# Performance work log

Measured on AMD Instinct MI355X. Metric: run time of the kernel, lower is better.

Reference implementation:

```python
import jax, jax.numpy as jnp
import numpy as np

EPS = 1e-5
CHUNK = 256
N_LAYERS = 4
D_MODEL = 1024
D_INNER = 2048
D_HEAD = 64
N_HEADS = 32
D_STATE = 64
D_CONV = 4
CONV_DIM = D_INNER + 2 * D_STATE  # ngroups=1
D_IN_PROJ = 2 * D_INNER + 2 * D_STATE + N_HEADS


def silu(x):
    return x * jax.nn.sigmoid(x)


def rmsnorm(x, w):
    return x * jax.lax.rsqrt(jnp.mean(x * x, axis=-1, keepdims=True) + EPS) * w


def segsum(x):
    # x: [..., T] -> [..., T, T] lower-triangular segment sums, -inf above diag
    T = x.shape[-1]
    cs = jnp.cumsum(x, axis=-1)
    ss = cs[..., :, None] - cs[..., None, :]
    mask = jnp.tril(jnp.ones((T, T), dtype=bool))
    return jnp.where(mask, ss, -jnp.inf)


def ssd(X, A, B, C, chunk):
    # X: [b,l,h,p] (already scaled by dt), A: [b,l,h] (= dt * A_head), B,C: [b,l,n] (ngroups=1)
    b, l, h, p = X.shape
    c = l // chunk
    X = X.reshape(b, c, chunk, h, p)
    A = A.reshape(b, c, chunk, h).transpose(0, 3, 1, 2)  # [b,h,c,l]
    B = B.reshape(b, c, chunk, -1)
    C = C.reshape(b, c, chunk, -1)
    Acs = jnp.cumsum(A, axis=-1)  # [b,h,c,l]
    # intra-chunk (diagonal blocks)
    Lm = jnp.exp(segsum(A))  # [b,h,c,l,l]
    Y_diag = jnp.einsum('bcln,bcsn,bhcls,bcshp->bclhp', C, B, Lm, X)
    # chunk end states
    decay_states = jnp.exp(Acs[..., -1:] - Acs)  # [b,h,c,l]
    states = jnp.einsum('bcln,bhcl,bclhp->bchpn', B, decay_states, X)
    # inter-chunk recurrence (c is small -> dense segsum over chunks)
    A_last = jnp.pad(Acs[..., -1], ((0, 0), (0, 0), (1, 0)))  # [b,h,c+1]
    decay_chunk = jnp.exp(segsum(A_last))  # [b,h,c+1,c+1]
    states = jnp.concatenate([jnp.zeros_like(states[:, :1]), states], axis=1)
    new_states = jnp.einsum('bhzc,bchpn->bzhpn', decay_chunk, states)
    states = new_states[:, :-1]  # state entering each chunk
    Y_off = jnp.einsum('bcln,bchpn,bhcl->bclhp', C, states, jnp.exp(Acs))
    return (Y_diag + Y_off).reshape(b, l, h, p)


def mamba2_layer(x, in_w, conv_w, conv_b, dt_bias, A_log, D, gnorm_w, out_w):
    b, l, _ = x.shape
    zxbcdt = jnp.einsum('bld,ed->ble', x, in_w)  # [b,l,D_IN_PROJ]
    z = zxbcdt[..., :D_INNER]
    xBC = zxbcdt[..., D_INNER:D_INNER + CONV_DIM]
    dt = zxbcdt[..., D_INNER + CONV_DIM:]  # [b,l,h]
    # depthwise causal conv1d + silu
    xpad = jnp.pad(xBC, ((0, 0), (D_CONV - 1, 0), (0, 0)))
    xconv = conv_b
    for k in range(D_CONV):
        xconv = xconv + xpad[:, k:k + l, :] * conv_w[:, k]
    xBC = silu(xconv)
    x_in = xBC[..., :D_INNER]
    B = xBC[..., D_INNER:D_INNER + D_STATE]
    C = xBC[..., D_INNER + D_STATE:]
    dt = jax.nn.softplus(dt + dt_bias)  # [b,l,h]
    A = -jnp.exp(A_log)  # [h]
    X = x_in.reshape(b, l, N_HEADS, D_HEAD)
    y = ssd(X * dt[..., None], dt * A, B, C, CHUNK)
    y = y + D[None, None, :, None] * X
    y = y.reshape(b, l, D_INNER)
    y = rmsnorm(y * silu(z), gnorm_w)
    return jnp.einsum('ble,de->bld', y, out_w)


def setup_inputs() -> dict:
    key = jax.random.key(0)
    ks = jax.random.split(key, 8)
    x = jax.random.normal(ks[0], (2, 2048, D_MODEL), dtype=jnp.float32)
    in_proj_w = jax.random.normal(ks[1], (N_LAYERS, D_IN_PROJ, D_MODEL), dtype=jnp.float32) * 0.02
    conv_w = jax.random.uniform(ks[2], (N_LAYERS, CONV_DIM, D_CONV), dtype=jnp.float32, minval=-0.5, maxval=0.5)
    conv_b = jnp.zeros((N_LAYERS, CONV_DIM), dtype=jnp.float32)
    A_log = jnp.log(jax.random.uniform(ks[3], (N_LAYERS, N_HEADS), dtype=jnp.float32, minval=1.0, maxval=16.0))
    dt0 = jax.random.uniform(ks[4], (N_LAYERS, N_HEADS), dtype=jnp.float32, minval=0.001, maxval=0.1)
    dt_bias = dt0 + jnp.log(-jnp.expm1(-dt0))  # inverse softplus
    D = jnp.ones((N_LAYERS, N_HEADS), dtype=jnp.float32)
    gnorm_w = jnp.ones((N_LAYERS, D_INNER), dtype=jnp.float32)
    out_proj_w = jax.random.normal(ks[5], (N_LAYERS, D_MODEL, D_INNER), dtype=jnp.float32) * 0.02
    rms_w = jnp.ones((N_LAYERS, D_MODEL), dtype=jnp.float32)
    return {"x": x, "in_proj_w": in_proj_w, "conv_w": conv_w, "conv_b": conv_b,
            "dt_bias": dt_bias, "A_log": A_log, "D": D, "gnorm_w": gnorm_w,
            "out_proj_w": out_proj_w, "rms_w": rms_w}


def reference(x, in_proj_w, conv_w, conv_b, dt_bias, A_log, D, gnorm_w, out_proj_w, rms_w):
    for i in range(N_LAYERS):
        x = x + mamba2_layer(rmsnorm(x, rms_w[i]), in_proj_w[i], conv_w[i], conv_b[i],
                             dt_bias[i], A_log[i], D[i], gnorm_w[i], out_proj_w[i])
    return x
```

## Files before the change

kernel.cpp:

```cpp
#include <hip/hip_runtime.h>
#include <cmath>

#define BATCH 2
#define LSEQ 2048
#define DMODEL 1024
#define DINNER 2048
#define NHEADS 32
#define DHEAD 64
#define DSTATE 64
#define DCONV 4
#define CONVDIM (DINNER + 2*DSTATE)
#define DINPROJ (2*DINNER + 2*DSTATE + NHEADS)
#define DINPROJ_PAD 4352
#define CHUNKSZ 256
#define NCHUNK (LSEQ/CHUNKSZ)
#define MROWS (BATCH*LSEQ)
#define EPSF 1e-5f

typedef __attribute__((ext_vector_type(8))) short shortx8;
typedef __attribute__((ext_vector_type(4))) short shortx4;
typedef __attribute__((ext_vector_type(4))) float floatx4;

__device__ __forceinline__ ushort f2bf(float f) {
  unsigned u = __float_as_uint(f);
  unsigned r = (u + 0x7fffu + ((u >> 16) & 1u)) >> 16;
  return (ushort)r;
}
__device__ __forceinline__ float bf2f(ushort b) {
  return __uint_as_float(((unsigned)b) << 16);
}

__device__ __forceinline__ shortx8 pack8(float4 a, float4 b) {
  shortx8 r;
  r[0] = (short)f2bf(a.x); r[1] = (short)f2bf(a.y);
  r[2] = (short)f2bf(a.z); r[3] = (short)f2bf(a.w);
  r[4] = (short)f2bf(b.x); r[5] = (short)f2bf(b.y);
  r[6] = (short)f2bf(b.z); r[7] = (short)f2bf(b.w);
  return r;
}

__device__ __forceinline__ void async_load16(const void* g, void* l) {
  __builtin_amdgcn_global_load_lds(
      (const __attribute__((address_space(1))) void*)g,
      (__attribute__((address_space(3))) void*)l, 16, 0, 0);
}

__device__ __forceinline__ float block_reduce_sum_256(float v, float* sb) {
  for (int off = 32; off > 0; off >>= 1) v += __shfl_down(v, off, 64);
  int lane = threadIdx.x & 63, wid = threadIdx.x >> 6;
  if (lane == 0) sb[wid] = v;
  __syncthreads();
  return sb[0] + sb[1] + sb[2] + sb[3];
}

__global__ __launch_bounds__(256) void cvt_bf16_k(const float* __restrict__ src,
                                                  ushort* __restrict__ dst,
                                                  size_t n_src, size_t n_dst) {
  size_t i = (size_t)blockIdx.x * 256 + threadIdx.x;
  if (i >= n_dst) return;
  float v = (i < n_src) ? src[i] : 0.f;
  dst[i] = f2bf(v);
}

__global__ __launch_bounds__(256) void cvt_w_all(const float* __restrict__ in_w,
                                                 const float* __restrict__ out_w,
                                                 ushort* __restrict__ in_bf,
                                                 ushort* __restrict__ out_bf) {
  unsigned g = (blockIdx.x * 256u + threadIdx.x) * 8u;
  const unsigned PL = (unsigned)DINPROJ_PAD * DMODEL;
  const unsigned n1 = 4u * PL;
  const unsigned n2 = 4u * DMODEL * DINNER;
  if (g < n1) {
    unsigned layer = g / PL, rem = g % PL;
    unsigned row = rem / DMODEL, col = rem % DMODEL;
    shortx8 o;
    if (row < DINPROJ) {
      const float* sp = in_w + ((size_t)layer * DINPROJ + row) * DMODEL + col;
      float4 a = *(const float4*)sp;
      float4 b = *(const float4*)(sp + 4);
      o = pack8(a, b);
    } else {
#pragma unroll
      for (int j = 0; j < 8; j++) o[j] = 0;
    }
    *(shortx8*)(in_bf + g) = o;
  } else if (g < n1 + n2) {
    unsigned j = g - n1;
    const float* sp = out_w + j;
    float4 a = *(const float4*)sp;
    float4 b = *(const float4*)(sp + 4);
    *(shortx8*)(out_bf + j) = pack8(a, b);
  }
}

__global__ __launch_bounds__(256) void rmsnorm_k(const float* __restrict__ x,
                                                 const float* __restrict__ w,
                                                 ushort* __restrict__ out) {
  __shared__ float sb[4];
  int r = blockIdx.x;
  const float* xr = x + (size_t)r * DMODEL;
  ushort* orow = out + (size_t)r * DMODEL;
  int c0 = threadIdx.x * 4;
  float4 v4 = *(const float4*)(xr + c0);
  float ssq = v4.x * v4.x + v4.y * v4.y + v4.z * v4.z + v4.w * v4.w;
  float s = block_reduce_sum_256(ssq, sb);
  float sc = rsqrtf(s / (float)DMODEL + EPSF);
  float4 w4 = *(const float4*)(w + c0);
  shortx4 o;
  o[0] = (short)f2bf(v4.x * sc * w4.x);
  o[1] = (short)f2bf(v4.y * sc * w4.y);
  o[2] = (short)f2bf(v4.z * sc * w4.z);
  o[3] = (short)f2bf(v4.w * sc * w4.w);
  *(shortx4*)(orow + c0) = o;
}

__device__ __forceinline__ void stage_tile(const ushort* __restrict__ A,
                                           const ushort* __restrict__ B,
                                           char* lb, int m0, int n0, int K, int k0,
                                           int wid, int rA, int sA) {
#pragma unroll
  for (int rd = 0; rd < 2; rd++) {
    int r = rd * 64 + rA;
    int sl = sA ^ ((r ^ (r >> 2)) & 3);
    async_load16(A + (size_t)(m0 + r) * K + (k0 + sl * 8), lb + rd * 4096 + wid * 1024);
  }
#pragma unroll
  for (int rd = 0; rd < 2; rd++) {
    int r = rd * 64 + rA;
    int sl = sA ^ ((r ^ (r >> 2)) & 3);
    async_load16(B + (size_t)(n0 + r) * K + (k0 + sl * 8), lb + 8192 + rd * 4096 + wid * 1024);
  }
}

__global__ __launch_bounds__(256, 3) void gemm_nt_mfma_pipe(
    const ushort* __restrict__ A, const ushort* __restrict__ B,
    ushort* __restrict__ Cbf, int M, int N, int K,
    int nbx, int rw, int rh) {
  __shared__ __align__(16) char lds[3][16384];
  int tid = threadIdx.x;
  int wid = tid >> 6, lane = tid & 63;
  int quad = lane >> 4, lrow = lane & 15;

  int d = blockIdx.x;
  int xcd = d & 7, wi = d >> 3;
  int ra = nbx / rw;
  int rn = xcd % ra, rm = xcd / ra;
  int bx = rn * rw + wi % rw;
  int by = rm * rh + wi / rw;

  int m0 = by * 128, n0 = bx * 128;
  int wm = (wid >> 1) * 64, wn = (wid & 1) * 64;
  int rA = tid >> 2, sA = tid & 3;

  floatx4 acc[4][4];
#pragma unroll
  for (int i = 0; i < 4; i++)
#pragma unroll
    for (int j = 0; j < 4; j++) acc[i][j] = (floatx4){0.f, 0.f, 0.f, 0.f};

  int NT = K >> 5;
#pragma unroll
  for (int t = 0; t < 2; t++)
    stage_tile(A, B, lds[t], m0, n0, K, t * 32, wid, rA, sA);

  int cur = 0, sb = 2;
  for (int t = 0; t < NT; t++) {
    if (t < NT - 1) asm volatile("s_waitcnt vmcnt(4)" ::: "memory");
    else            asm volatile("s_waitcnt vmcnt(0)" ::: "memory");
    __builtin_amdgcn_s_barrier();
    __builtin_amdgcn_sched_barrier(0);
    if (t + 2 < NT) {
      stage_tile(A, B, lds[sb], m0, n0, K, (t + 2) * 32, wid, rA, sA);
      sb = (sb == 2) ? 0 : sb + 1;
    }

    const char* Ab = lds[cur];
    const char* Bb = Ab + 8192;
    cur = (cur == 2) ? 0 : cur + 1;
    shortx8 af[4], bfr[4];
#pragma unroll
    for (int i = 0; i < 4; i++) {
      int r = wm + i * 16 + lrow;
      af[i] = *(const shortx8*)(Ab + r * 64 + ((quad ^ ((r ^ (r >> 2)) & 3)) << 4));
    }
#pragma unroll
    for (int j = 0; j < 4; j++) {
      int r = wn + j * 16 + lrow;
      bfr[j] = *(const shortx8*)(Bb + r * 64 + ((quad ^ ((r ^ (r >> 2)) & 3)) << 4));
    }
    __builtin_amdgcn_s_setprio(1);
#pragma unroll
    for (int i = 0; i < 4; i++)
#pragma unroll
      for (int j = 0; j < 4; j++)
        acc[i][j] = __builtin_amdgcn_mfma_f32_16x16x32_bf16(af[i], bfr[j], acc[i][j], 0, 0, 0);
    __builtin_amdgcn_s_setprio(0);
  }

#pragma unroll
  for (int i = 0; i < 4; i++) {
    int r0 = m0 + wm + i * 16 + quad * 4;
#pragma unroll
    for (int j = 0; j < 4; j++) {
      int n = n0 + wn + j * 16 + lrow;
      if (n < N)
#pragma unroll
        for (int r = 0; r < 4; r++)
          Cbf[(size_t)(r0 + r) * N + n] = f2bf(acc[i][j][r]);
    }
  }
}

__device__ __forceinline__ void stage_tile64(const ushort* __restrict__ A,
                                             const ushort* __restrict__ B,
                                             char* lb, int m0, int n0, int K, int k0,
                                             int wid, int rA, int sA) {
#pragma unroll
  for (int rd = 0; rd < 2; rd++) {
    int r = rd * 64 + rA;
    int sl = sA ^ ((r ^ (r >> 2)) & 3);
    async_load16(A + (size_t)(m0 + r) * K + (k0 + sl * 8), lb + rd * 4096 + wid * 1024);
  }
  {
    int r = rA;
    int sl = sA ^ ((r ^ (r >> 2)) & 3);
    async_load16(B + (size_t)(n0 + r) * K + (k0 + sl * 8), lb + 8192 + wid * 1024);
  }
}

__global__ __launch_bounds__(256, 2) void gemm_nt_64(
    const ushort* __restrict__ A, const ushort* __restrict__ B,
    float* __restrict__ C, const float* __restrict__ resid,
    int M, int N, int K, int nbx, int rw, int rh) {
  __shared__ __align__(16) char lds[3][12288];
  int tid = threadIdx.x;
  int wid = tid >> 6, lane = tid & 63;
  int quad = lane >> 4, lrow = lane & 15;

  int d = blockIdx.x;
  int xcd = d & 7, wi = d >> 3;
  int ra = nbx / rw;
  int rn = xcd % ra, rm = xcd / ra;
  int bx = rn * rw + wi % rw;
  int by = rm * rh + wi / rw;

  int m0 = by * 128, n0 = bx * 64;
  int wm = (wid >> 1) * 64, wn = (wid & 1) * 32;
  int rA = tid >> 2, sA = tid & 3;

  floatx4 acc[4][2];
#pragma unroll
  for (int i = 0; i < 4; i++)
#pragma unroll
    for (int j = 0; j < 2; j++) acc[i][j] = (floatx4){0.f, 0.f, 0.f, 0.f};

  int NT = K >> 5;
#pragma unroll
  for (int t = 0; t < 2; t++)
    stage_tile64(A, B, lds[t], m0, n0, K, t * 32, wid, rA, sA);

  int cur = 0, sb = 2;
  for (int t = 0; t < NT; t++) {
    if (t < NT - 1) asm volatile("s_waitcnt vmcnt(3)" ::: "memory");
    else            asm volatile("s_waitcnt vmcnt(0)" ::: "memory");
    __builtin_amdgcn_s_barrier();
    __builtin_amdgcn_sched_barrier(0);
    if (t + 2 < NT) {
      stage_tile64(A, B, lds[sb], m0, n0, K, (t + 2) * 32, wid, rA, sA);
      sb = (sb == 2) ? 0 : sb + 1;
    }

    const char* Ab = lds[cur];
    const char* Bb = Ab + 8192;
    cur = (cur == 2) ? 0 : cur + 1;
    shortx8 af[4], bfr[2];
#pragma unroll
    for (int i = 0; i < 4; i++) {
      int r = wm + i * 16 + lrow;
      af[i] = *(const shortx8*)(Ab + r * 64 + ((quad ^ ((r ^ (r >> 2)) & 3)) << 4));
    }
#pragma unroll
    for (int j = 0; j < 2; j++) {
      int r = wn + j * 16 + lrow;
      bfr[j] = *(const shortx8*)(Bb + r * 64 + ((quad ^ ((r ^ (r >> 2)) & 3)) << 4));
    }
    __builtin_amdgcn_s_setprio(1);
#pragma unroll
    for (int i = 0; i < 4; i++)
#pragma unroll
      for (int j = 0; j < 2; j++)
        acc[i][j] = __builtin_amdgcn_mfma_f32_16x16x32_bf16(af[i], bfr[j], acc[i][j], 0, 0, 0);
    __builtin_amdgcn_s_setprio(0);
  }

  bool hasR = (resid != nullptr);
#pragma unroll
  for (int i = 0; i < 4; i++) {
    int r0 = m0 + wm + i * 16 + quad * 4;
#pragma unroll
    for (int j = 0; j < 2; j++) {
      int n = n0 + wn + j * 16 + lrow;
#pragma unroll
      for (int r = 0; r < 4; r++) {
        size_t idx = (size_t)(r0 + r) * N + n;
        float v = acc[i][j][r];
        if (hasR) v += resid[idx];
        C[idx] = v;
      }
    }
  }
}

__global__ __launch_bounds__(256) void convcum_k(const ushort* __restrict__ zxbf,
                                                 const float* __restrict__ cw,
                                                 const float* __restrict__ cb,
                                                 ushort* __restrict__ xbf,
                                                 const float* __restrict__ dt_bias,
                                                 const float* __restrict__ A_log,
                                                 float* __restrict__ dt_sp,
                                                 float* __restrict__ dtA_cs) {
  __shared__ float buf[256];
  int tid = threadIdx.x;
  if (blockIdx.x < MROWS / 8) {
    int r0 = blockIdx.x * 8;
    int bstart = r0 & ~(LSEQ - 1);
#pragma unroll
    for (int rep = 0; rep < 2; rep++) {
      int ch;
      if (rep == 0) ch = tid * 8;
      else { if (tid >= (CONVDIM - 2048) / 8) break; ch = 2048 + tid * 8; }
      float wv[8][4], bias[8];
#pragma unroll
      for (int j = 0; j < 8; j++) {
        float4 w4 = *(const float4*)(cw + (ch + j) * 4);
        wv[j][0] = w4.x; wv[j][1] = w4.y; wv[j][2] = w4.z; wv[j][3] = w4.w;
        bias[j] = cb[ch + j];
      }
      float xw[11][8];
#pragma unroll
      for (int wr = 0; wr < 11; wr++) {
        int rr = r0 - 3 + wr;
        if (rr < bstart) {
#pragma unroll
          for (int j = 0; j < 8; j++) xw[wr][j] = 0.f;
        } else {
          shortx8 v = *(const shortx8*)(zxbf + (size_t)rr * DINPROJ + DINNER + ch);
#pragma unroll
          for (int j = 0; j < 8; j++) xw[wr][j] = bf2f((ushort)v[j]);
        }
      }
#pragma unroll
      for (int o = 0; o < 8; o++) {
        shortx8 ov;
#pragma unroll
        for (int j = 0; j < 8; j++) {
          float acc = bias[j];
#pragma unroll
          for (int k = 0; k < 4; k++) acc += xw[o + k][j] * wv[j][k];
          float s = acc / (1.f + expf(-acc));
          ov[j] = (short)f2bf(s);
        }
        *(shortx8*)(xbf + (size_t)(r0 + o) * CONVDIM + ch) = ov;
      }
    }
  } else {
    int bid = blockIdx.x - MROWS / 8;
    int h = bid & 31, c = (bid >> 5) & 7, b = bid >> 8;
    int l = tid;
    float Aneg = -expf(A_log[h]);
    int row = b * LSEQ + c * CHUNKSZ + l;
    float v = bf2f(zxbf[(size_t)row * DINPROJ + DINNER + CONVDIM + h]) + dt_bias[h];
    float dtv = (v > 20.f) ? v : log1pf(expf(v));
    dt_sp[row * 32 + h] = dtv;
    buf[l] = dtv * Aneg;
    __syncthreads();
    for (int off = 1; off < 256; off <<= 1) {
      float add = (l >= off) ? buf[l - off] : 0.f;
      __syncthreads();
      buf[l] += add;
      __syncthreads();
    }
    dtA_cs[(size_t)bid * CHUNKSZ + l] = buf[l];
  }
}

#define ST_STRIDE 72
__global__ __launch_bounds__(256) void states_mfma(const ushort* __restrict__ xbf,
                                                   const float* __restrict__ dt_sp,
                                                   const float* __restrict__ dtA_cs,
                                                   float* __restrict__ st_raw) {
  __shared__ ushort XT[64 * ST_STRIDE];
  __shared__ ushort BT[64 * ST_STRIDE];
  __shared__ float wrow[64];
  int bid = blockIdx.x;
  int h = bid & 31, c = (bid >> 5) & 7, b = bid >> 8;
  int tid = threadIdx.x;
  int w = tid >> 6, lane = tid & 63;
  int quad = lane >> 4, lrow = lane & 15;
  int cbase = bid * CHUNKSZ;
  int rowbase = b * LSEQ + c * CHUNKSZ;
  float T = dtA_cs[cbase + CHUNKSZ - 1];
  floatx4 acc[4];
  for (int jt = 0; jt < 4; jt++) acc[jt] = (floatx4){0.f, 0.f, 0.f, 0.f};
  int row_l = tid >> 2, seg = tid & 3;
  for (int lt = 0; lt < 4; lt++) {
    __syncthreads();
    if (tid < 64) {
      int row = rowbase + lt * 64 + tid;
      wrow[tid] = dt_sp[row * 32 + h] * __expf(T - dtA_cs[cbase + lt * 64 + tid]);
    }
    __syncthreads();
    {
      int row = rowbase + lt * 64 + row_l;
      const ushort* bp = xbf + (size_t)row * CONVDIM + DINNER + seg * 16;
      const ushort* xp = xbf + (size_t)row * CONVDIM + h * DHEAD + seg * 16;
      shortx8 b0 = *(const shortx8*)bp;
      shortx8 b1 = *(const shortx8*)(bp + 8);
      shortx8 x0 = *(const shortx8*)xp;
      shortx8 x1 = *(const shortx8*)(xp + 8);
      float wv = wrow[row_l];
#pragma unroll
      for (int j = 0; j < 8; j++) {
        int c0 = seg * 16 + j;
        int c1 = c0 + 8;
        int k0 = ((c0 >> 1) & 7) << 3;
        int k1 = ((c1 >> 1) & 7) << 3;
        BT[c0 * ST_STRIDE + (row_l ^ k0)] = (ushort)b0[j];
        BT[c1 * ST_STRIDE + (row_l ^ k1)] = (ushort)b1[j];
        XT[c0 * ST_STRIDE + (row_l ^ k0)] = f2bf(bf2f((ushort)x0[j]) * wv);
        XT[c1 * ST_STRIDE + (row_l ^ k1)] = f2bf(bf2f((ushort)x1[j]) * wv);
      }
    }
    __syncthreads();
    int arow = w * 16 + lrow;
    int akey = ((arow >> 1) & 7) << 3;
    for (int kk = 0; kk < 64; kk += 32) {
      shortx8 af = *(const shortx8*)&XT[arow * ST_STRIDE + ((kk + quad * 8) ^ akey)];
      for (int jt = 0; jt < 4; jt++) {
        int brow = jt * 16 + lrow;
        int bkey = ((brow >> 1) & 7) << 3;
        shortx8 bf = *(const shortx8*)&BT[brow * ST_STRIDE + ((kk + quad * 8) ^ bkey)];
        acc[jt] = __builtin_amdgcn_mfma_f32_16x16x32_bf16(af, bf, acc[jt], 0, 0, 0);
      }
    }
  }
  size_t base = (size_t)bid * (DHEAD * DSTATE);
  for (int jt = 0; jt < 4; jt++) {
    int n = jt * 16 + lrow;
    for (int r = 0; r < 4; r++) {
      int p = w * 16 + quad * 4 + r;
      st_raw[base + (size_t)p * 64 + n] = acc[jt][r];
    }
  }
}

__global__ __launch_bounds__(256) void scan_k(float* __restrict__ st,
                                              const float* __restrict__ dtA_cs) {
  int bid = blockIdx.x;
  int seg = bid & 3, h = (bid >> 2) & 31, b = bid >> 7;
  int tid = threadIdx.x;
  int off = seg * 1024;
  float s[4];
  for (int i = 0; i < 4; i++) s[i] = 0.f;
  for (int c = 0; c < NCHUNK; c++) {
    int g = (b * NCHUNK + c) * 32 + h;
    float dec = expf(dtA_cs[(size_t)g * CHUNKSZ + CHUNKSZ - 1]);
    size_t base = (size_t)g * (DHEAD * DSTATE) + off;
    for (int i = 0; i < 4; i++) {
      int idx = tid + i * 256;
      float raw = st[base + idx];
      st[base + idx] = s[i];
      s[i] = s[i] * dec + raw;
    }
  }
}

#define BS_STRIDE 72
#define XT_STRIDE 68
#define PW_STRIDE 72
__global__ __launch_bounds__(256) void ydiag_mfma(const ushort* __restrict__ xbf,
                                                  const float* __restrict__ dt_sp,
                                                  const float* __restrict__ dtA_cs,
                                                  const float* __restrict__ st_in,
                                                  ushort* __restrict__ Y) {
  __shared__ ushort Bs[64 * BS_STRIDE];
  __shared__ ushort XsT[64 * XT_STRIDE];
  __shared__ ushort Pw[4 * 16 * PW_STRIDE];
  __shared__ float cs[256];
  int tid = threadIdx.x;
  int w = tid >> 6, lane = tid & 63;
  int quad = lane >> 4, lrow = lane & 15;
  int bid = blockIdx.x;
  int lt = bid & 3, h = (bid >> 2) & 31, c = (bid >> 7) & 7, b = bid >> 10;
  int g = (b * NCHUNK + c) * 32 + h;
  int cbase = g * CHUNKSZ;
  int rowbase = b * LSEQ + c * CHUNKSZ;

  cs[tid] = dtA_cs[cbase + tid];
  __syncthreads();

  int mrow = lt * 64 + w * 16;
  float csl[4];
  for (int r = 0; r < 4; r++) csl[r] = cs[mrow + quad * 4 + r];

  shortx8 Cf[2];
  {
    const ushort* cp = xbf + (size_t)(rowbase + mrow + lrow) * CONVDIM + DINNER + DSTATE;
    for (int q = 0; q < 2; q++)
      Cf[q] = *(const shortx8*)(cp + q * 32 + quad * 8);
  }

  floatx4 acc[4];
  for (int jt = 0; jt < 4; jt++) acc[jt] = (floatx4){0.f, 0.f, 0.f, 0.f};
  const float* stp = st_in + (size_t)g * (DHEAD * DSTATE);
  for (int q = 0; q < 2; q++) {
    for (int jt = 0; jt < 4; jt++) {
      const float* sp = stp + (size_t)(jt * 16 + lrow) * 64 + q * 32 + quad * 8;
      shortx8 sf = pack8(*(const float4*)sp, *(const float4*)(sp + 4));
      acc[jt] = __builtin_amdgcn_mfma_f32_16x16x32_bf16(Cf[q], sf, acc[jt], 0, 0, 0);
    }
  }
  for (int jt = 0; jt < 4; jt++)
    for (int r = 0; r < 4; r++) acc[jt][r] *= __expf(csl[r]);

  ushort* myP = Pw + w * 16 * PW_STRIDE;
  int row_l = tid >> 2, seg = tid & 3;
  for (int st = 0; st <= lt; st++) {
    __syncthreads();
    {
      int row = rowbase + st * 64 + row_l;
      const ushort* bp = xbf + (size_t)row * CONVDIM + DINNER + seg * 16;
      const ushort* xp = xbf + (size_t)row * CONVDIM + h * DHEAD + seg * 16;
      shortx8 b0 = *(const shortx8*)bp;
      shortx8 b1 = *(const shortx8*)(bp + 8);
      shortx8 x0 = *(const shortx8*)xp;
      shortx8 x1 = *(const shortx8*)(xp + 8);
      float dtv = dt_sp[row * 32 + h];
      *(shortx8*)&Bs[row_l * BS_STRIDE + seg * 16] = b0;
      *(shortx8*)&Bs[row_l * BS_STRIDE + seg * 16 + 8] = b1;
#pragma unroll
      for (int j = 0; j < 8; j++) {
        int c0 = seg * 16 + j;
        XsT[c0 * XT_STRIDE + row_l]       = f2bf(bf2f((ushort)x0[j]) * dtv);
        XsT[(c0 + 8) * XT_STRIDE + row_l] = f2bf(bf2f((ushort)x1[j]) * dtv);
      }
    }
    __syncthreads();
    for (int jt = 0; jt < 4; jt++) {
      floatx4 s = (floatx4){0.f, 0.f, 0.f, 0.f};
      for (int q = 0; q < 2; q++) {
        shortx8 bfr = *(const shortx8*)&Bs[(jt * 16 + lrow) * BS_STRIDE + q * 32 + quad * 8];
        s = __builtin_amdgcn_mfma_f32_16x16x32_bf16(Cf[q], bfr, s, 0, 0, 0);
      }
      int scol = st * 64 + jt * 16 + lrow;
      float css = cs[scol];
      for (int r = 0; r < 4; r++) {
        int l = mrow + quad * 4 + r;
        float v = (scol <= l) ? s[r] * __expf(csl[r] - css) : 0.f;
        myP[(quad * 4 + r) * PW_STRIDE + jt * 16 + lrow] = f2bf(v);
      }
    }
    shortx8 pf[2];
    for (int q = 0; q < 2; q++)
      pf[q] = *(const shortx8*)&myP[lrow * PW_STRIDE + q * 32 + quad * 8];
    for (int jt = 0; jt < 4; jt++) {
      for (int q = 0; q < 2; q++) {
        const ushort* xp = &XsT[(jt * 16 + lrow) * XT_STRIDE + q * 32 + quad * 8];
        shortx4 lo = *(const shortx4*)xp;
        shortx4 hi = *(const shortx4*)(xp + 4);
        shortx8 xf = __builtin_shufflevector(lo, hi, 0, 1, 2, 3, 4, 5, 6, 7);
        acc[jt] = __builtin_amdgcn_mfma_f32_16x16x32_bf16(pf[q], xf, acc[jt], 0, 0, 0);
      }
    }
  }
  int growb = rowbase + mrow + quad * 4;
  for (int jt = 0; jt < 4; jt++)
    for (int r = 0; r < 4; r++)
      Y[(size_t)(growb + r) * DINNER + h * DHEAD + jt * 16 + lrow] = f2bf(acc[jt][r]);
}

__global__ __launch_bounds__(256) void gatenorm_k(const ushort* __restrict__ Ybf,
                                                  const ushort* __restrict__ zxbf,
                                                  const ushort* __restrict__ xbf,
                                                  const float* __restrict__ Dvec,
                                                  const float* __restrict__ gw,
                                                  ushort* __restrict__ obf) {
  __shared__ float sb[4];
  int r = blockIdx.x;
  int c0 = threadIdx.x * 8;
  const ushort* yr = Ybf + (size_t)r * DINNER;
  const ushort* zr = zxbf + (size_t)r * DINPROJ;
  const ushort* xr = xbf + (size_t)r * CONVDIM;
  ushort* orow = obf + (size_t)r * DINNER;
  shortx8 y8 = *(const shortx8*)(yr + c0);
  shortx8 z8 = *(const shortx8*)(zr + c0);
  shortx8 x8 = *(const shortx8*)(xr + c0);
  float Dv = Dvec[threadIdx.x >> 3];
  float t[8]; float ssq = 0.f;
#pragma unroll
  for (int i = 0; i < 8; i++) {
    float z = bf2f((ushort)z8[i]);
    float yv = bf2f((ushort)y8[i]) + Dv * bf2f((ushort)x8[i]);
    float gv = yv * (z / (1.f + expf(-z)));
    t[i] = gv;
    ssq += gv * gv;
  }
  float s = block_reduce_sum_256(ssq, sb);
  float sc = rsqrtf(s / (float)DINNER + EPSF);
  float4 g0 = *(const float4*)(gw + c0);
  float4 g1 = *(const float4*)(gw + c0 + 4);
  shortx8 o;
  o[0] = (short)f2bf(t[0] * sc * g0.x); o[1] = (short)f2bf(t[1] * sc * g0.y);
  o[2] = (short)f2bf(t[2] * sc * g0.z); o[3] = (short)f2bf(t[3] * sc * g0.w);
  o[4] = (short)f2bf(t[4] * sc * g1.x); o[5] = (short)f2bf(t[5] * sc * g1.y);
  o[6] = (short)f2bf(t[6] * sc * g1.z); o[7] = (short)f2bf(t[7] * sc * g1.w);
  *(shortx8*)(orow + c0) = o;
}

extern "C" void kernel_launch(void* const* d_in, const int* in_sizes, int n_in,
                              void* d_out, int out_size, void* d_ws, size_t ws_size,
                              hipStream_t stream) {
  const float* x_in     = (const float*)d_in[0];
  const float* in_w     = (const float*)d_in[1];
  const float* conv_w   = (const float*)d_in[2];
  const float* conv_b   = (const float*)d_in[3];
  const float* dt_bias  = (const float*)d_in[4];
  const float* A_log    = (const float*)d_in[5];
  const float* Dvec     = (const float*)d_in[6];
  const float* gnorm_w  = (const float*)d_in[7];
  const float* out_w    = (const float*)d_in[8];
  const float* rms_w    = (const float*)d_in[9];
  float* out = (float*)d_out;

  float* ws = (float*)d_ws;
  size_t o = 0;
  float* x_cur  = ws + o; o += (size_t)MROWS * DMODEL;
  ushort* zx_bf = (ushort*)(ws + o); o += (size_t)MROWS * DINPROJ / 2;
  ushort* xbf   = (ushort*)(ws + o); o += (size_t)MROWS * CONVDIM / 2;
  float* dt_sp  = ws + o; o += (size_t)MROWS * NHEADS;
  float* dtA_cs = ws + o; o += (size_t)BATCH * NCHUNK * NHEADS * CHUNKSZ;
  float* st     = ws + o; o += (size_t)BATCH * NCHUNK * NHEADS * DHEAD * DSTATE;
  ushort* Ybf   = (ushort*)(ws + o); o += (size_t)MROWS * DINNER / 2;
  ushort* act_bf = (ushort*)(ws + o); o += (size_t)MROWS * DINNER / 2;
  size_t base_f = o;

  size_t inw_f  = (size_t)4 * DINPROJ_PAD * DMODEL / 2;
  size_t outw_f = (size_t)4 * DMODEL * DINNER / 2;
  bool hoist = ws_size >= (base_f + inw_f + outw_f) * sizeof(float);

  ushort* in_bf_all = (ushort*)(ws + base_f);
  ushort* out_bf_all = (ushort*)(ws + base_f + inw_f);
  ushort* w_bf_fb = (ushort*)(ws + base_f);

  hipMemcpyAsync(x_cur, x_in, (size_t)MROWS * DMODEL * sizeof(float),
                 hipMemcpyDeviceToDevice, stream);

  if (hoist) {
    unsigned ntot = (4u * DINPROJ_PAD * DMODEL + 4u * DMODEL * DINNER) / 8u;
    cvt_w_all<<<(ntot + 255) / 256, 256, 0, stream>>>(in_w, out_w, in_bf_all, out_bf_all);
  }

  for (int i = 0; i < 4; i++) {
    const float* conv_w_i = conv_w  + (size_t)i * CONVDIM * DCONV;
    const float* conv_b_i = conv_b  + (size_t)i * CONVDIM;
    const float* dtb_i    = dt_bias + (size_t)i * NHEADS;
    const float* Alog_i   = A_log   + (size_t)i * NHEADS;
    const float* D_i      = Dvec    + (size_t)i * NHEADS;
    const float* gw_i     = gnorm_w + (size_t)i * DINNER;
    const float* rms_w_i  = rms_w   + (size_t)i * DMODEL;

    const ushort* w1_bf;
    const ushort* w2_bf;
    if (hoist) {
      w1_bf = in_bf_all  + (size_t)i * DINPROJ_PAD * DMODEL;
      w2_bf = out_bf_all + (size_t)i * DMODEL * DINNER;
    } else {
      size_t ns = (size_t)DINPROJ * DMODEL, nd = (size_t)DINPROJ_PAD * DMODEL;
      cvt_bf16_k<<<(nd + 255) / 256, 256, 0, stream>>>(
          in_w + (size_t)i * DINPROJ * DMODEL, w_bf_fb, ns, nd);
      w1_bf = w_bf_fb;
      w2_bf = w_bf_fb;
    }

    rmsnorm_k<<<MROWS, 256, 0, stream>>>(x_cur, rms_w_i, act_bf);
    gemm_nt_mfma_pipe<<<(DINPROJ_PAD / 128) * (MROWS / 128), 256, 0, stream>>>(
        act_bf, w1_bf, zx_bf, MROWS, DINPROJ, DMODEL, DINPROJ_PAD / 128, 17, 8);
    convcum_k<<<MROWS / 8 + BATCH * NCHUNK * NHEADS, 256, 0, stream>>>(
        zx_bf, conv_w_i, conv_b_i, xbf, dtb_i, Alog_i, dt_sp, dtA_cs);
    states_mfma<<<BATCH * NCHUNK * NHEADS, 256, 0, stream>>>(xbf, dt_sp, dtA_cs, st);
    scan_k<<<BATCH * NHEADS * 4, 256, 0, stream>>>(st, dtA_cs);
    ydiag_mfma<<<BATCH * NCHUNK * NHEADS * 4, 256, 0, stream>>>(
        xbf, dt_sp, dtA_cs, st, Ybf);
    gatenorm_k<<<MROWS, 256, 0, stream>>>(Ybf, zx_bf, xbf, D_i, gw_i, act_bf);
    if (!hoist) {
      size_t ns = (size_t)DMODEL * DINNER;
      cvt_bf16_k<<<(ns + 255) / 256, 256, 0, stream>>>(
          out_w + (size_t)i * DMODEL * DINNER, (ushort*)w_bf_fb, ns, ns);
    }
    float* outC = (i == 3) ? out : x_cur;
    gemm_nt_64<<<(MROWS / 128) * (DMODEL / 64), 256, 0, stream>>>(
        act_bf, w2_bf, outC, x_cur, MROWS, DMODEL, DINNER, DMODEL / 64, 8, 8);
  }
}
```

Baseline: 868.6 us.

## Merge ydiag row tiles into one block per chunk-head to reuse B/X staging

The ydiag kernel previously launched four blocks per (batch, chunk, head), one per 64-row tile, each restaging B and dt-scaled X tiles into shared memory. Now one block processes all four row tiles, loading each B/X source tile once and applying it to every causal row tile. This removes redundant global loads and conversions but quadruples accumulator registers (64 floatx4 values plus C fragments), cuts the grid from 2048 to 512 blocks, and serialises more work per block, which may lower occupancy.

```diff
diff --git a/kernel.cpp b/kernel.cpp
--- a/kernel.cpp
+++ b/kernel.cpp
@@ -491,7 +491,7 @@
   int w = tid >> 6, lane = tid & 63;
   int quad = lane >> 4, lrow = lane & 15;
   int bid = blockIdx.x;
-  int lt = bid & 3, h = (bid >> 2) & 31, c = (bid >> 7) & 7, b = bid >> 10;
+  int h = bid & 31, c = (bid >> 5) & 7, b = bid >> 8;
   int g = (b * NCHUNK + c) * 32 + h;
   int cbase = g * CHUNKSZ;
   int rowbase = b * LSEQ + c * CHUNKSZ;
@@ -499,33 +499,43 @@
   cs[tid] = dtA_cs[cbase + tid];
   __syncthreads();
 
-  int mrow = lt * 64 + w * 16;
-  float csl[4];
-  for (int r = 0; r < 4; r++) csl[r] = cs[mrow + quad * 4 + r];
-
-  shortx8 Cf[2];
-  {
+  shortx8 Cf[4][2];
+  float csl[4][4];
+  floatx4 acc[4][4];
+#pragma unroll
+  for (int mt = 0; mt < 4; mt++) {
+    int mrow = mt * 64 + w * 16;
+#pragma unroll
+    for (int r = 0; r < 4; r++) csl[mt][r] = cs[mrow + quad * 4 + r];
     const ushort* cp = xbf + (size_t)(rowbase + mrow + lrow) * CONVDIM + DINNER + DSTATE;
-    for (int q = 0; q < 2; q++)
-      Cf[q] = *(const shortx8*)(cp + q * 32 + quad * 8);
-  }
-
-  floatx4 acc[4];
-  for (int jt = 0; jt < 4; jt++) acc[jt] = (floatx4){0.f, 0.f, 0.f, 0.f};
+#pragma unroll
+    for (int q = 0; q < 2; q++) Cf[mt][q] = *(const shortx8*)(cp + q * 32 + quad * 8);
+#pragma unroll
+    for (int jt = 0; jt < 4; jt++) acc[mt][jt] = (floatx4){0.f, 0.f, 0.f, 0.f};
+  }
+
   const float* stp = st_in + (size_t)g * (DHEAD * DSTATE);
+#pragma unroll
   for (int q = 0; q < 2; q++) {
+#pragma unroll
     for (int jt = 0; jt < 4; jt++) {
       const float* sp = stp + (size_t)(jt * 16 + lrow) * 64 + q * 32 + quad * 8;
       shortx8 sf = pack8(*(const float4*)sp, *(const float4*)(sp + 4));
-      acc[jt] = __builtin_amdgcn_mfma_f32_16x16x32_bf16(Cf[q], sf, acc[jt], 0, 0, 0);
-    }
-  }
-  for (int jt = 0; jt < 4; jt++)
-    for (int r = 0; r < 4; r++) acc[jt][r] *= __expf(csl[r]);
+#pragma unroll
+      for (int mt = 0; mt < 4; mt++)
+        acc[mt][jt] = __builtin_amdgcn_mfma_f32_16x16x32_bf16(Cf[mt][q], sf, acc[mt][jt], 0, 0, 0);
+    }
+  }
+#pragma unroll
+  for (int mt = 0; mt < 4; mt++)
+#pragma unroll
+    for (int jt = 0; jt < 4; jt++)
+#pragma unroll
+      for (int r = 0; r < 4; r++) acc[mt][jt][r] *= __expf(csl[mt][r]);
 
   ushort* myP = Pw + w * 16 * PW_STRIDE;
   int row_l = tid >> 2, seg = tid & 3;
-  for (int st = 0; st <= lt; st++) {
+  for (int st = 0; st < 4; st++) {
     __syncthreads();
     {
       int row = rowbase + st * 64 + row_l;
@@ -546,37 +556,53 @@
       }
     }
     __syncthreads();
-    for (int jt = 0; jt < 4; jt++) {
-      floatx4 s = (floatx4){0.f, 0.f, 0.f, 0.f};
-      for (int q = 0; q < 2; q++) {
-        shortx8 bfr = *(const shortx8*)&Bs[(jt * 16 + lrow) * BS_STRIDE + q * 32 + quad * 8];
-        s = __builtin_amdgcn_mfma_f32_16x16x32_bf16(Cf[q], bfr, s, 0, 0, 0);
-      }
-      int scol = st * 64 + jt * 16 + lrow;
-      float css = cs[scol];
-      for (int r = 0; r < 4; r++) {
-        int l = mrow + quad * 4 + r;
-        float v = (scol <= l) ? s[r] * __expf(csl[r] - css) : 0.f;
-        myP[(quad * 4 + r) * PW_STRIDE + jt * 16 + lrow] = f2bf(v);
-      }
-    }
-    shortx8 pf[2];
-    for (int q = 0; q < 2; q++)
-      pf[q] = *(const shortx8*)&myP[lrow * PW_STRIDE + q * 32 + quad * 8];
-    for (int jt = 0; jt < 4; jt++) {
-      for (int q = 0; q < 2; q++) {
-        const ushort* xp = &XsT[(jt * 16 + lrow) * XT_STRIDE + q * 32 + quad * 8];
-        shortx4 lo = *(const shortx4*)xp;
-        shortx4 hi = *(const shortx4*)(xp + 4);
-        shortx8 xf = __builtin_shufflevector(lo, hi, 0, 1, 2, 3, 4, 5, 6, 7);
-        acc[jt] = __builtin_amdgcn_mfma_f32_16x16x32_bf16(pf[q], xf, acc[jt], 0, 0, 0);
-      }
-    }
-  }
-  int growb = rowbase + mrow + quad * 4;
-  for (int jt = 0; jt < 4; jt++)
-    for (int r = 0; r < 4; r++)
-      Y[(size_t)(growb + r) * DINNER + h * DHEAD + jt * 16 + lrow] = f2bf(acc[jt][r]);
+#pragma unroll
+    for (int mt = 0; mt < 4; mt++) {
+      if (mt < st) continue;
+#pragma unroll
+      for (int jt = 0; jt < 4; jt++) {
+        floatx4 s = (floatx4){0.f, 0.f, 0.f, 0.f};
+#pragma unroll
+        for (int q = 0; q < 2; q++) {
+          shortx8 bfr = *(const shortx8*)&Bs[(jt * 16 + lrow) * BS_STRIDE + q * 32 + quad * 8];
+          s = __builtin_amdgcn_mfma_f32_16x16x32_bf16(Cf[mt][q], bfr, s, 0, 0, 0);
+        }
+        int scol = st * 64 + jt * 16 + lrow;
+        float css = cs[scol];
+#pragma unroll
+        for (int r = 0; r < 4; r++) {
+          int l = mt * 64 + w * 16 + quad * 4 + r;
+          float v = (scol <= l) ? s[r] * __expf(csl[mt][r] - css) : 0.f;
+          myP[(quad * 4 + r) * PW_STRIDE + jt * 16 + lrow] = f2bf(v);
+        }
+      }
+      shortx8 pf[2];
+#pragma unroll
+      for (int q = 0; q < 2; q++)
+        pf[q] = *(const shortx8*)&myP[lrow * PW_STRIDE + q * 32 + quad * 8];
+#pragma unroll
+      for (int jt = 0; jt < 4; jt++) {
+#pragma unroll
+        for (int q = 0; q < 2; q++) {
+          const ushort* xp = &XsT[(jt * 16 + lrow) * XT_STRIDE + q * 32 + quad * 8];
+          shortx4 lo = *(const shortx4*)xp;
+          shortx4 hi = *(const shortx4*)(xp + 4);
+          shortx8 xf = __builtin_shufflevector(lo, hi, 0, 1, 2, 3, 4, 5, 6, 7);
+          acc[mt][jt] = __builtin_amdgcn_mfma_f32_16x16x32_bf16(pf[q], xf, acc[mt][jt], 0, 0, 0);
+        }
+      }
+    }
+  }
+
+#pragma unroll
+  for (int mt = 0; mt < 4; mt++) {
+    int growb = rowbase + mt * 64 + w * 16 + quad * 4;
+#pragma unroll
+    for (int jt = 0; jt < 4; jt++)
+#pragma unroll
+      for (int r = 0; r < 4; r++)
+        Y[(size_t)(growb + r) * DINNER + h * DHEAD + jt * 16 + lrow] = f2bf(acc[mt][jt][r]);
+  }
 }
 
 __global__ __launch_bounds__(256) void gatenorm_k(const ushort* __restrict__ Ybf,
@@ -689,7 +715,7 @@
         zx_bf, conv_w_i, conv_b_i, xbf, dtb_i, Alog_i, dt_sp, dtA_cs);
     states_mfma<<<BATCH * NCHUNK * NHEADS, 256, 0, stream>>>(xbf, dt_sp, dtA_cs, st);
     scan_k<<<BATCH * NHEADS * 4, 256, 0, stream>>>(st, dtA_cs);
-    ydiag_mfma<<<BATCH * NCHUNK * NHEADS * 4, 256, 0, stream>>>(
+    ydiag_mfma<<<BATCH * NCHUNK * NHEADS, 256, 0, stream>>>(
         xbf, dt_sp, dtA_cs, st, Ybf);
     gatenorm_k<<<MROWS, 256, 0, stream>>>(Ybf, zx_bf, xbf, D_i, gw_i, act_bf);
     if (!hoist) {
```

After: 937.1 us. 7.9% more time.
